# Performance work log

Measured on AMD Instinct MI355X. Metric: run time of the kernel, lower is better.

The kernel has to match this reference:

```python
import jax, jax.numpy as jnp
import numpy as np

N = 50000      # nodes (B*N flattened)
E = 800000     # edges
IN = 128       # in_channels
HID = 32       # hidden_channels per head
HEADS = 2
OUT = 64       # out_channels
NEG_SLOPE = 0.2


def setup_inputs() -> dict:
    key = jax.random.key(0)
    ks = jax.random.split(key, 10)
    x = jax.random.normal(ks[0], (N, IN), jnp.float32)
    edge_index = jax.random.randint(ks[1], (2, E), 0, N, dtype=jnp.int64)
    s = 0.1
    W1 = jax.random.normal(ks[2], (IN, HEADS * HID), jnp.float32) * s
    a_src1 = jax.random.normal(ks[3], (HEADS, HID), jnp.float32) * s
    a_dst1 = jax.random.normal(ks[4], (HEADS, HID), jnp.float32) * s
    b1 = jnp.zeros((HEADS * HID,), jnp.float32)
    W2 = jax.random.normal(ks[5], (HEADS * HID, OUT), jnp.float32) * s
    a_src2 = jax.random.normal(ks[6], (1, OUT), jnp.float32) * s
    a_dst2 = jax.random.normal(ks[7], (1, OUT), jnp.float32) * s
    b2 = jnp.zeros((OUT,), jnp.float32)
    return {"x": x, "edge_index": edge_index,
            "W1": W1, "a_src1": a_src1, "a_dst1": a_dst1, "b1": b1,
            "W2": W2, "a_src2": a_src2, "a_dst2": a_dst2, "b2": b2}


def gat_conv(x, src, dst, W, a_s, a_d, b, heads, ch, concat):
    """PyG GATConv: per-edge attention, softmax over incoming edges of dst."""
    n = x.shape[0]
    h = (x @ W).reshape(n, heads, ch)                       # [N,H,C]
    al_s = (h * a_s).sum(-1)                                # [N,H]
    al_d = (h * a_d).sum(-1)                                # [N,H]
    e = jax.nn.leaky_relu(al_s[src] + al_d[dst], NEG_SLOPE)  # [E,H]
    e_max = jax.ops.segment_max(e, dst, num_segments=n)     # [N,H]
    ex = jnp.exp(e - e_max[dst])
    denom = jax.ops.segment_sum(ex, dst, num_segments=n)
    coef = ex / (denom[dst] + 1e-16)                         # [E,H]
    out = jax.ops.segment_sum(h[src] * coef[:, :, None], dst, num_segments=n)  # [N,H,C]
    out = out.reshape(n, heads * ch) if concat else out.mean(axis=1)
    return out + b


def reference(x, edge_index, W1, a_src1, a_dst1, b1, W2, a_src2, a_dst2, b2):
    loops = jnp.arange(N, dtype=edge_index.dtype)
    src = jnp.concatenate([edge_index[0], loops])  # add_self_loops=True (PyG default)
    dst = jnp.concatenate([edge_index[1], loops])
    h1 = jax.nn.relu(gat_conv(x, src, dst, W1, a_src1, a_dst1, b1, HEADS, HID, True))
    return gat_conv(h1, src, dst, W2, a_src2, a_dst2, b2, 1, OUT, False)
```

## Files before the change

### kernel.cpp

```cpp
#include <hip/hip_runtime.h>

#define IN_CH   128
#define HIDX    64
#define NEG_SLOPE 0.2f
#define CAP     64
#define BNODES  32
#define NXCD    8
#define SUB     4
#define NSEGT   (NXCD * SUB)
#define SEGCAP  64

static inline size_t align256(size_t x) { return (x + 255) & ~(size_t)255; }

__device__ inline unsigned pk_bf16(float a, float b) {
    unsigned ua = __float_as_uint(a), ub = __float_as_uint(b);
    ua = (ua + 0x7FFFu + ((ua >> 16) & 1u)) >> 16;
    ub = (ub + 0x7FFFu + ((ub >> 16) & 1u)) >> 16;
    return ua | (ub << 16);
}

__global__ void k_zero(int* __restrict__ p, int n) {
    int i = blockIdx.x * blockDim.x + threadIdx.x;
    if (i < n) p[i] = 0;
}

__global__ void k_bucket(const int* __restrict__ ei, int E, int NBUK,
                         int* __restrict__ bcnt, unsigned* __restrict__ bkt) {
    int t = blockIdx.x * blockDim.x + threadIdx.x;
    int i = t * 2;
    if (i >= E) return;
    unsigned xcd;
    asm volatile("s_getreg_b32 %0, hwreg(HW_REG_XCC_ID)" : "=s"(xcd));
    xcd &= (NXCD - 1);
    const int xb = (int)xcd * (NBUK * SUB);
    const int2 sv = *(const int2*)(ei + i);
    const int2 dv = *(const int2*)(ei + E + i);
#pragma unroll
    for (int u = 0; u < 2; ++u) {
        const int s = (u == 0) ? sv.x : sv.y;
        const int d = (u == 0) ? dv.x : dv.y;
        const int slot = xb + (d >> 5) * SUB + ((t + u) & (SUB - 1));
        int pos = atomicAdd(&bcnt[slot], 1);
        if (pos < SEGCAP)
            bkt[(size_t)slot * SEGCAP + pos] =
                ((unsigned)(d & (BNODES - 1)) << 16) | (unsigned)s;
    }
}

template <int K, int H, bool RELU_IN>
__global__ __launch_bounds__(256)
void k_gemm(const float* __restrict__ X, const float* __restrict__ W,
            const float* __restrict__ bin,
            const float* __restrict__ a_s, const float* __restrict__ a_d,
            unsigned short* __restrict__ HoutB,
            float* __restrict__ als, float* __restrict__ ald, int N) {
    constexpr int STR = 68;
    __shared__ float Wl[K * 64];
    __shared__ float xT[K * STR];

    const int t  = threadIdx.x;
    const int nb = blockIdx.x * 64;

    {
        const float4* W4 = (const float4*)W;
        float4* Wl4 = (float4*)Wl;
#pragma unroll
        for (int i = 0; i < (K * 16) / 256; ++i)
            Wl4[i * 256 + t] = W4[i * 256 + t];
    }
    {
        constexpr int QK = K / 4;
        constexpr int RS = 256 / QK;
        const int kq = t % QK;
        const int r0 = t / QK;
        for (int n = r0; n < 64; n += RS) {
            const int node = nb + n;
            const int cn = node < N ? node : N - 1;
            float4 v = *(const float4*)(X + (size_t)cn * K + kq * 4);
            if (RELU_IN) {
                const float4 bv = *(const float4*)(bin + kq * 4);
                v.x = fmaxf(v.x + bv.x, 0.f);
                v.y = fmaxf(v.y + bv.y, 0.f);
                v.z = fmaxf(v.z + bv.z, 0.f);
                v.w = fmaxf(v.w + bv.w, 0.f);
            }
            const int ns = (((n >> 2) ^ (kq & 7)) << 2) + (n & 3);
            xT[(kq * 4 + 0) * STR + ns] = v.x;
            xT[(kq * 4 + 1) * STR + ns] = v.y;
            xT[(kq * 4 + 2) * STR + ns] = v.z;
            xT[(kq * 4 + 3) * STR + ns] = v.w;
        }
    }
    __syncthreads();

    const int cg = t & 15;
    const int ng = t >> 4;

    float acc[4][4] = {{0.f}};
#pragma unroll 4
    for (int k = 0; k < K; ++k) {
        const int xb = ((ng ^ ((k >> 2) & 7)) << 2);
        const float4 xv = *(const float4*)&xT[k * STR + xb];
        const float4 wv = *(const float4*)&Wl[k * 64 + (cg << 2)];
        acc[0][0] += xv.x * wv.x; acc[0][1] += xv.x * wv.y;
        acc[0][2] += xv.x * wv.z; acc[0][3] += xv.x * wv.w;
        acc[1][0] += xv.y * wv.x; acc[1][1] += xv.y * wv.y;
        acc[1][2] += xv.y * wv.z; acc[1][3] += xv.y * wv.w;
        acc[2][0] += xv.z * wv.x; acc[2][1] += xv.z * wv.y;
        acc[2][2] += xv.z * wv.z; acc[2][3] += xv.z * wv.w;
        acc[3][0] += xv.w * wv.x; acc[3][1] += xv.w * wv.y;
        acc[3][2] += xv.w * wv.z; acc[3][3] += xv.w * wv.w;
    }

    const float4 asv = *(const float4*)(a_s + cg * 4);
    const float4 adv = *(const float4*)(a_d + cg * 4);
#pragma unroll
    for (int i = 0; i < 4; ++i) {
        const int node = nb + ng * 4 + i;
        float ps = acc[i][0] * asv.x + acc[i][1] * asv.y +
                   acc[i][2] * asv.z + acc[i][3] * asv.w;
        float pd = acc[i][0] * adv.x + acc[i][1] * adv.y +
                   acc[i][2] * adv.z + acc[i][3] * adv.w;
#pragma unroll
        for (int m = 1; m < (H == 2 ? 8 : 16); m <<= 1) {
            ps += __shfl_xor(ps, m, 64);
            pd += __shfl_xor(pd, m, 64);
        }
        if (node < N) {
            uint2 pv;
            pv.x = pk_bf16(acc[i][0], acc[i][1]);
            pv.y = pk_bf16(acc[i][2], acc[i][3]);
            *(uint2*)(HoutB + (size_t)node * 64 + cg * 4) = pv;
            if (H == 2) {
                if ((cg & 7) == 0) {
                    als[node * 2 + (cg >> 3)] = ps;
                    ald[node * 2 + (cg >> 3)] = pd;
                }
            } else if (cg == 0) {
                als[node] = ps;
                ald[node] = pd;
            }
        }
    }
}

template <int H>
__device__ inline void agg_walk(
    int node, int deg, const unsigned short* __restrict__ lst, bool lds,
    const float* __restrict__ als, float aldh, int head, int g, int cl,
    const unsigned short* __restrict__ hB, const float* __restrict__ bias,
    float* __restrict__ out) {
    float4 a0 = make_float4(0.f, 0.f, 0.f, 0.f);
    float4 a1 = make_float4(0.f, 0.f, 0.f, 0.f);
    float dsum = 0.f;

    auto accum = [&](int s, float c) {
        const uint4 u = *(const uint4*)(hB + (size_t)s * 64 + cl * 8);
        a0.x += c * __uint_as_float(u.x << 16);
        a0.y += c * __uint_as_float(u.x & 0xFFFF0000u);
        a0.z += c * __uint_as_float(u.y << 16);
        a0.w += c * __uint_as_float(u.y & 0xFFFF0000u);
        a1.x += c * __uint_as_float(u.z << 16);
        a1.y += c * __uint_as_float(u.z & 0xFFFF0000u);
        a1.z += c * __uint_as_float(u.w << 16);
        a1.w += c * __uint_as_float(u.w & 0xFFFF0000u);
    };

    if (g == 0) {
        float e = als[node * H + head] + aldh;
        e = e > 0.f ? e : NEG_SLOPE * e;
        const float c = __expf(e);
        dsum = c;
        accum(node, c);
    }
#pragma unroll 2
    for (int j = g; j < deg; j += 8) {
        const int s = lst[j];
        float e = als[s * H + head] + aldh;
        e = e > 0.f ? e : NEG_SLOPE * e;
        const float c = __expf(e);
        dsum += c;
        accum(s, c);
    }
#pragma unroll
    for (int m = 8; m < 64; m <<= 1) {
        a0.x += __shfl_xor(a0.x, m, 64); a0.y += __shfl_xor(a0.y, m, 64);
        a0.z += __shfl_xor(a0.z, m, 64); a0.w += __shfl_xor(a0.w, m, 64);
        a1.x += __shfl_xor(a1.x, m, 64); a1.y += __shfl_xor(a1.y, m, 64);
        a1.z += __shfl_xor(a1.z, m, 64); a1.w += __shfl_xor(a1.w, m, 64);
        dsum  += __shfl_xor(dsum,  m, 64);
    }
    if (g == 0) {
        const float inv = 1.0f / (dsum + 1e-16f);
        a0.x *= inv; a0.y *= inv; a0.z *= inv; a0.w *= inv;
        a1.x *= inv; a1.y *= inv; a1.z *= inv; a1.w *= inv;
        if (bias) {
            const float4* bp = (const float4*)(bias + cl * 8);
            const float4 b0 = bp[0], b1v = bp[1];
            a0.x += b0.x;  a0.y += b0.y;  a0.z += b0.z;  a0.w += b0.w;
            a1.x += b1v.x; a1.y += b1v.y; a1.z += b1v.z; a1.w += b1v.w;
        }
        float4* op = (float4*)(out + (size_t)node * 64 + cl * 8);
        op[0] = a0; op[1] = a1;
    }
    (void)lds;
}

template <int H>
__global__ __launch_bounds__(256)
void k_aggf(const int* __restrict__ bcnt, const unsigned* __restrict__ bkt,
            int N, int NBUK, int* __restrict__ cnt,
            unsigned short* __restrict__ csrf,
            const float* __restrict__ als, const float* __restrict__ ald,
            const unsigned short* __restrict__ hB,
            const float* __restrict__ bias, float* __restrict__ out) {
    __shared__ unsigned short ls[BNODES * CAP];
    __shared__ int lcnt[BNODES];
    const int b = blockIdx.x;
    const int t = threadIdx.x;
    const int w = t >> 6, lane = t & 63;
    const int nb = b * BNODES;

    if (t < BNODES) lcnt[t] = 0;
    __syncthreads();

    for (int seg = w; seg < NSEGT; seg += 4) {
        const int slot = (seg >> 2) * (NBUK * SUB) + b * SUB + (seg & 3);
        int m = bcnt[slot]; if (m > SEGCAP) m = SEGCAP;
        const unsigned* sp = bkt + (size_t)slot * SEGCAP;
        for (int i = lane; i < m; i += 64) {
            const unsigned v = sp[i];
            const int dl = v >> 16;
            const int r  = atomicAdd(&lcnt[dl], 1);
            if (r < CAP) ls[dl * CAP + r] = (unsigned short)(v & 0xFFFF);
        }
    }
    __syncthreads();

    ((uint4*)(csrf + (size_t)nb * CAP))[t] = ((const uint4*)ls)[t];
    if (t < BNODES && nb + t < N) {
        const int c = lcnt[t];
        cnt[nb + t] = c < CAP ? c : CAP;
    }

    const int g  = lane >> 3;
    const int cl = lane & 7;
    const int head = (H == 2) ? (cl >> 2) : 0;
#pragma unroll
    for (int k = 0; k < 8; ++k) {
        const int dl = w * 8 + k;
        const int node = nb + dl;
        if (node >= N) break;
        int deg = lcnt[dl]; if (deg > CAP) deg = CAP;
        const float aldh = ald[node * H + head];
        agg_walk<H>(node, deg, ls + dl * CAP, true,
                    als, aldh, head, g, cl, hB, bias, out);
    }
}

template <int H>
__global__ __launch_bounds__(256)
void k_agg(const int* __restrict__ cnt, const unsigned short* __restrict__ csrf,
           const float* __restrict__ als, const float* __restrict__ ald,
           const unsigned short* __restrict__ hB,
           const float* __restrict__ bias, float* __restrict__ out, int N) {
    int wid = blockIdx.x * 4 + (threadIdx.x >> 6);
    int lane = threadIdx.x & 63;
    if (wid >= N) return;
    const int deg = cnt[wid];
    const int g  = lane >> 3;
    const int cl = lane & 7;
    const int head = (H == 2) ? (cl >> 2) : 0;
    const float aldh = ald[wid * H + head];
    agg_walk<H>(wid, deg, csrf + (size_t)wid * CAP, false,
                als, aldh, head, g, cl, hB, bias, out);
}

extern "C" void kernel_launch(void* const* d_in, const int* in_sizes, int n_in,
                              void* d_out, int out_size, void* d_ws, size_t ws_size,
                              hipStream_t stream) {
    const float* x   = (const float*)d_in[0];
    const int*   ei  = (const int*)d_in[1];
    const float* W1  = (const float*)d_in[2];
    const float* as1 = (const float*)d_in[3];
    const float* ad1 = (const float*)d_in[4];
    const float* b1  = (const float*)d_in[5];
    const float* W2  = (const float*)d_in[6];
    const float* as2 = (const float*)d_in[7];
    const float* ad2 = (const float*)d_in[8];
    const float* b2  = (const float*)d_in[9];
    float* out = (float*)d_out;

    const int N    = in_sizes[0] / IN_CH;
    const int E    = in_sizes[1] / 2;
    const int NBUK = (N + BNODES - 1) / BNODES;
    const int NCTR = NBUK * NSEGT;

    char* ws = (char*)d_ws;
    size_t o = 0;
    auto alloc = [&](size_t bytes) { void* p = ws + o; o = align256(o + bytes); return p; };
    int*            cnt  = (int*)alloc((size_t)N * sizeof(int));
    int*            bcnt = (int*)alloc((size_t)NCTR * sizeof(int));
    unsigned*       bkt  = (unsigned*)alloc((size_t)NCTR * SEGCAP * sizeof(unsigned));
    unsigned short* csrf = (unsigned short*)alloc((size_t)NBUK * BNODES * CAP * sizeof(unsigned short));
    unsigned short* hb   = (unsigned short*)alloc((size_t)N * 64 * sizeof(unsigned short));
    float*          als1 = (float*)alloc((size_t)N * 2 * sizeof(float));
    float*          ald1 = (float*)alloc((size_t)N * 2 * sizeof(float));
    float*          als2 = (float*)alloc((size_t)N * sizeof(float));
    float*          ald2 = (float*)alloc((size_t)N * sizeof(float));
    float*          out1 = out;

    k_zero<<<(NCTR + 255) / 256, 256, 0, stream>>>(bcnt, NCTR);
    k_bucket<<<(E / 2 + 255) / 256, 256, 0, stream>>>(ei, E, NBUK, bcnt, bkt);

    const int gg = (N + 63) / 64;
    const int gn = (N + 3) / 4;

    k_gemm<IN_CH, 2, false><<<gg, 256, 0, stream>>>(
        x, W1, nullptr, as1, ad1, hb, als1, ald1, N);
    k_aggf<2><<<NBUK, 256, 0, stream>>>(
        bcnt, bkt, N, NBUK, cnt, csrf, als1, ald1, hb, nullptr, out1);

    k_gemm<HIDX, 1, true><<<gg, 256, 0, stream>>>(
        out1, W2, b1, as2, ad2, hb, als2, ald2, N);
    k_agg<1><<<gn, 256, 0, stream>>>(
        cnt, csrf, als2, ald2, hb, b2, out, N);
}
```

Before: 138.5 us.

## Fuse layer-2 linear transform and attention logits into layer-1 aggregation kernel

Layer-1 aggregation results are now kept in shared memory, and the same block applies bias+ReLU, multiplies by W2 staged in LDS, and writes the bf16 layer-2 features and attention logits. This removes one kernel launch and the global write and re-read of the layer-1 output. In exchange the aggregation kernel uses more LDS (about 25 KB extra), which may lower occupancy, and it needs a separate hb2 buffer.

```diff
diff --git a/kernel.cpp b/kernel.cpp
--- a/kernel.cpp
+++ b/kernel.cpp
@@ -9,6 +9,7 @@
 #define SUB     4
 #define NSEGT   (NXCD * SUB)
 #define SEGCAP  64
+#define OSTR    68
 
 static inline size_t align256(size_t x) { return (x + 255) & ~(size_t)255; }
 
@@ -47,10 +48,9 @@
     }
 }
 
-template <int K, int H, bool RELU_IN>
+template <int K, int H>
 __global__ __launch_bounds__(256)
 void k_gemm(const float* __restrict__ X, const float* __restrict__ W,
-            const float* __restrict__ bin,
             const float* __restrict__ a_s, const float* __restrict__ a_d,
             unsigned short* __restrict__ HoutB,
             float* __restrict__ als, float* __restrict__ ald, int N) {
@@ -77,13 +77,6 @@
             const int node = nb + n;
             const int cn = node < N ? node : N - 1;
             float4 v = *(const float4*)(X + (size_t)cn * K + kq * 4);
-            if (RELU_IN) {
-                const float4 bv = *(const float4*)(bin + kq * 4);
-                v.x = fmaxf(v.x + bv.x, 0.f);
-                v.y = fmaxf(v.y + bv.y, 0.f);
-                v.z = fmaxf(v.z + bv.z, 0.f);
-                v.w = fmaxf(v.w + bv.w, 0.f);
-            }
             const int ns = (((n >> 2) ^ (kq & 7)) << 2) + (n & 3);
             xT[(kq * 4 + 0) * STR + ns] = v.x;
             xT[(kq * 4 + 1) * STR + ns] = v.y;
@@ -146,10 +139,10 @@
 
 template <int H>
 __device__ inline void agg_walk(
-    int node, int deg, const unsigned short* __restrict__ lst, bool lds,
+    int node, int deg, const unsigned short* __restrict__ lst,
     const float* __restrict__ als, float aldh, int head, int g, int cl,
     const unsigned short* __restrict__ hB, const float* __restrict__ bias,
-    float* __restrict__ out) {
+    float* __restrict__ dstrow) {
     float4 a0 = make_float4(0.f, 0.f, 0.f, 0.f);
     float4 a1 = make_float4(0.f, 0.f, 0.f, 0.f);
     float dsum = 0.f;
@@ -200,10 +193,9 @@
             a0.x += b0.x;  a0.y += b0.y;  a0.z += b0.z;  a0.w += b0.w;
             a1.x += b1v.x; a1.y += b1v.y; a1.z += b1v.z; a1.w += b1v.w;
         }
-        float4* op = (float4*)(out + (size_t)node * 64 + cl * 8);
+        float4* op = (float4*)(dstrow + cl * 8);
         op[0] = a0; op[1] = a1;
     }
-    (void)lds;
 }
 
 template <int H>
@@ -213,9 +205,15 @@
             unsigned short* __restrict__ csrf,
             const float* __restrict__ als, const float* __restrict__ ald,
             const unsigned short* __restrict__ hB,
-            const float* __restrict__ bias, float* __restrict__ out) {
+            const float* __restrict__ W2, const float* __restrict__ b1,
+            const float* __restrict__ as2, const float* __restrict__ ad2,
+            unsigned short* __restrict__ hb2,
+            float* __restrict__ als2, float* __restrict__ ald2) {
     __shared__ unsigned short ls[BNODES * CAP];
     __shared__ int lcnt[BNODES];
+    __shared__ float o1[BNODES * OSTR];
+    __shared__ float W2l[64 * 64];
+    __shared__ float b1l[64];
     const int b = blockIdx.x;
     const int t = threadIdx.x;
     const int w = t >> 6, lane = t & 63;
@@ -235,6 +233,13 @@
             if (r < CAP) ls[dl * CAP + r] = (unsigned short)(v & 0xFFFF);
         }
     }
+    {
+        const float4* W24 = (const float4*)W2;
+        float4* W2l4 = (float4*)W2l;
+#pragma unroll
+        for (int i = 0; i < 4; ++i) W2l4[i * 256 + t] = W24[i * 256 + t];
+        if (t < 16) ((float4*)b1l)[t] = ((const float4*)b1)[t];
+    }
     __syncthreads();
 
     ((uint4*)(csrf + (size_t)nb * CAP))[t] = ((const uint4*)ls)[t];
@@ -253,8 +258,49 @@
         if (node >= N) break;
         int deg = lcnt[dl]; if (deg > CAP) deg = CAP;
         const float aldh = ald[node * H + head];
-        agg_walk<H>(node, deg, ls + dl * CAP, true,
-                    als, aldh, head, g, cl, hB, bias, out);
+        agg_walk<H>(node, deg, ls + dl * CAP,
+                    als, aldh, head, g, cl, hB, nullptr, o1 + dl * OSTR);
+    }
+    __syncthreads();
+
+    {
+        const int n  = t >> 3;
+        const int c8 = t & 7;
+        const int node = nb + n;
+        float acc8[8] = {0.f};
+        const float* orow = o1 + n * OSTR;
+#pragma unroll 8
+        for (int k = 0; k < 64; ++k) {
+            const float v = fmaxf(orow[k] + b1l[k], 0.f);
+            const float4 w0 = *(const float4*)&W2l[k * 64 + c8 * 8];
+            const float4 w1 = *(const float4*)&W2l[k * 64 + c8 * 8 + 4];
+            acc8[0] += v * w0.x; acc8[1] += v * w0.y;
+            acc8[2] += v * w0.z; acc8[3] += v * w0.w;
+            acc8[4] += v * w1.x; acc8[5] += v * w1.y;
+            acc8[6] += v * w1.z; acc8[7] += v * w1.w;
+        }
+        const float4 s0 = *(const float4*)(as2 + c8 * 8);
+        const float4 s1 = *(const float4*)(as2 + c8 * 8 + 4);
+        const float4 d0 = *(const float4*)(ad2 + c8 * 8);
+        const float4 d1 = *(const float4*)(ad2 + c8 * 8 + 4);
+        float ps = acc8[0] * s0.x + acc8[1] * s0.y + acc8[2] * s0.z + acc8[3] * s0.w
+                 + acc8[4] * s1.x + acc8[5] * s1.y + acc8[6] * s1.z + acc8[7] * s1.w;
+        float pd = acc8[0] * d0.x + acc8[1] * d0.y + acc8[2] * d0.z + acc8[3] * d0.w
+                 + acc8[4] * d1.x + acc8[5] * d1.y + acc8[6] * d1.z + acc8[7] * d1.w;
+#pragma unroll
+        for (int m = 1; m < 8; m <<= 1) {
+            ps += __shfl_xor(ps, m, 64);
+            pd += __shfl_xor(pd, m, 64);
+        }
+        if (node < N) {
+            uint4 pv;
+            pv.x = pk_bf16(acc8[0], acc8[1]);
+            pv.y = pk_bf16(acc8[2], acc8[3]);
+            pv.z = pk_bf16(acc8[4], acc8[5]);
+            pv.w = pk_bf16(acc8[6], acc8[7]);
+            *(uint4*)(hb2 + (size_t)node * 64 + c8 * 8) = pv;
+            if (c8 == 0) { als2[node] = ps; ald2[node] = pd; }
+        }
     }
 }
 
@@ -272,8 +318,8 @@
     const int cl = lane & 7;
     const int head = (H == 2) ? (cl >> 2) : 0;
     const float aldh = ald[wid * H + head];
-    agg_walk<H>(wid, deg, csrf + (size_t)wid * CAP, false,
-                als, aldh, head, g, cl, hB, bias, out);
+    agg_walk<H>(wid, deg, csrf + (size_t)wid * CAP,
+                als, aldh, head, g, cl, hB, bias, out + (size_t)wid * 64);
 }
 
 extern "C" void kernel_launch(void* const* d_in, const int* in_sizes, int n_in,
@@ -304,11 +350,11 @@
     unsigned*       bkt  = (unsigned*)alloc((size_t)NCTR * SEGCAP * sizeof(unsigned));
     unsigned short* csrf = (unsigned short*)alloc((size_t)NBUK * BNODES * CAP * sizeof(unsigned short));
     unsigned short* hb   = (unsigned short*)alloc((size_t)N * 64 * sizeof(unsigned short));
+    unsigned short* hb2  = (unsigned short*)alloc((size_t)N * 64 * sizeof(unsigned short));
     float*          als1 = (float*)alloc((size_t)N * 2 * sizeof(float));
     float*          ald1 = (float*)alloc((size_t)N * 2 * sizeof(float));
     float*          als2 = (float*)alloc((size_t)N * sizeof(float));
     float*          ald2 = (float*)alloc((size_t)N * sizeof(float));
-    float*          out1 = out;
 
     k_zero<<<(NCTR + 255) / 256, 256, 0, stream>>>(bcnt, NCTR);
     k_bucket<<<(E / 2 + 255) / 256, 256, 0, stream>>>(ei, E, NBUK, bcnt, bkt);
@@ -316,13 +362,11 @@
     const int gg = (N + 63) / 64;
     const int gn = (N + 3) / 4;
 
-    k_gemm<IN_CH, 2, false><<<gg, 256, 0, stream>>>(
-        x, W1, nullptr, as1, ad1, hb, als1, ald1, N);
+    k_gemm<IN_CH, 2><<<gg, 256, 0, stream>>>(
+        x, W1, as1, ad1, hb, als1, ald1, N);
     k_aggf<2><<<NBUK, 256, 0, stream>>>(
-        bcnt, bkt, N, NBUK, cnt, csrf, als1, ald1, hb, nullptr, out1);
-
-    k_gemm<HIDX, 1, true><<<gg, 256, 0, stream>>>(
-        out1, W2, b1, as2, ad2, hb, als2, ald2, N);
+        bcnt, bkt, N, NBUK, cnt, csrf, als1, ald1, hb,
+        W2, b1, as2, ad2, hb2, als2, ald2);
     k_agg<1><<<gn, 256, 0, stream>>>(
-        cnt, csrf, als2, ald2, hb, b2, out, N);
-}
+        cnt, csrf, als2, ald2, hb2, b2, out, N);
+}
```

New measurement: 141.5 us. 2.1% more time.
